# Kernel tuning notes

Hardware: AMD Instinct MI355X
Metric: run time of the kernel (lower is better)

Reference implementation:

```python
import jax, jax.numpy as jnp
import numpy as np

B, N, DIN = 8192, 25, 256
H, F = 8, 32  # heads, per-head dim (output_dim // heads)
E = 48       # directed bone edges
NEG_SLOPE = 0.2


def setup_inputs() -> dict:
    key = jax.random.key(0)
    k0, k1, k2, k3, k4 = jax.random.split(key, 5)
    joint_embeddings = jax.random.normal(k0, (B, N, DIN), dtype=jnp.float32)
    W = jax.random.normal(k1, (DIN, H * F), dtype=jnp.float32) * (1.0 / np.sqrt(DIN))
    a_src = jax.random.normal(k2, (H, F), dtype=jnp.float32) * 0.1
    a_dst = jax.random.normal(k3, (H, F), dtype=jnp.float32) * 0.1
    bias = jnp.zeros((H * F,), dtype=jnp.float32)
    bone_edges = jax.random.randint(k4, (2, E), 0, N, dtype=jnp.int32)
    return {"joint_embeddings": joint_embeddings, "W": W, "a_src": a_src,
            "a_dst": a_dst, "bias": bias, "bone_edges": bone_edges}


def reference(joint_embeddings, W, a_src, a_dst, bias, bone_edges):
    # Linear projection per head: (B, N, H, F)
    h = (joint_embeddings @ W).reshape(B, N, H, F)
    # Per-node attention logits (GATConv splits a into src/dst halves)
    alpha_s = jnp.einsum('bnhf,hf->bnh', h, a_src)  # (B, N, H)
    alpha_d = jnp.einsum('bnhf,hf->bnh', h, a_dst)  # (B, N, H)
    # PyG GATConv default add_self_loops=True
    loops = jnp.arange(N, dtype=bone_edges.dtype)
    src = jnp.concatenate([bone_edges[0], loops])  # (E+N,)
    dst = jnp.concatenate([bone_edges[1], loops])  # (E+N,)
    # Per-edge scores, leaky relu
    e = jax.nn.leaky_relu(alpha_s[:, src] + alpha_d[:, dst], NEG_SLOPE)  # (B, Et, H)
    e_t = jnp.moveaxis(e, 1, 0)  # (Et, B, H) -- segment ops over leading axis
    # Numerically stable segment softmax over incoming edges of each dst node
    m = jax.ops.segment_max(e_t, dst, num_segments=N)  # (N, B, H)
    m = jnp.where(jnp.isfinite(m), m, 0.0)
    ex = jnp.exp(e_t - m[dst])
    denom = jax.ops.segment_sum(ex, dst, num_segments=N)  # (N, B, H)
    alpha = ex / (denom[dst] + 1e-16)  # (Et, B, H)
    # Scatter-aggregate messages
    h_nodes = jnp.moveaxis(h, 1, 0)           # (N, B, H, F)
    msgs = alpha[..., None] * h_nodes[src]     # (Et, B, H, F)
    out = jax.ops.segment_sum(msgs, dst, num_segments=N)  # (N, B, H, F)
    out = jnp.moveaxis(out, 0, 1).reshape(B, N, H * F) + bias
    return out
```

## Files before the change

### kernel.cpp

```cpp
#include <hip/hip_runtime.h>
#include <math.h>

#define NBATCH 8192
#define NNODE  25
#define DIN    256
#define NH     8
#define NF     32
#define HF     256
#define NE     48
#define NT     73
#define NEG_SLOPE 0.2f

#define WS_LNM_OFF 139264

typedef __bf16 bf16x8 __attribute__((ext_vector_type(8)));
typedef float  f32x4  __attribute__((ext_vector_type(4)));

static __device__ __forceinline__ unsigned short f2bf(float f) {
    unsigned int u = __float_as_uint(f);
    return (unsigned short)((u + 0x7fffu + ((u >> 16) & 1u)) >> 16);
}

static __device__ __forceinline__ float bpermf(int idxb, float v) {
    return __int_as_float(__builtin_amdgcn_ds_bpermute(idxb, __float_as_int(v)));
}

__global__ void prep(const float* __restrict__ W,
                     const float* __restrict__ a_src,
                     const float* __restrict__ a_dst,
                     const int*   __restrict__ edges,
                     unsigned short* __restrict__ wf,
                     float* __restrict__ lnm) {
    const int blk = blockIdx.x;
    if (blk < 34) {
        const int tid  = blk * 256 + threadIdx.x;
        const int lane = tid & 63;
        const int ks   = (tid >> 6) & 7;
        const int ct   = tid >> 9;
        const int k0   = ks * 32 + (lane >> 4) * 8;
        if (ct < 16) {
            const int col = ct * 16 + (lane & 15);
#pragma unroll
            for (int j = 0; j < 8; ++j)
                wf[tid * 8 + j] = f2bf(W[(k0 + j) * HF + col]);
        } else {
            const int hp = lane & 15;
            const float* av = (hp < 8) ? (a_src + hp * NF) : (a_dst + (hp - 8) * NF);
            const int wc = (hp & 7) * NF;
#pragma unroll
            for (int j = 0; j < 8; ++j) {
                float s = 0.f;
                for (int f = 0; f < NF; ++f)
                    s = fmaf(W[(k0 + j) * HF + wc + f], av[f], s);
                wf[tid * 8 + j] = f2bf(s);
            }
        }
    } else {
        __shared__ int cnt[32 * 32];
        const int t = threadIdx.x;
        for (int i = t; i < 1024; i += 256) cnt[i] = 0;
        __syncthreads();
        if (t < NT) {
            const int s = (t < NE) ? edges[t]      : (t - NE);
            const int d = (t < NE) ? edges[NE + t] : (t - NE);
            atomicAdd(&cnt[d * 32 + s], 1);
        }
        __syncthreads();
        for (int i = t; i < 1024; i += 256) {
            const int c = cnt[i];
            lnm[i] = (c > 0) ? logf((float)c) : -1e30f;
        }
    }
}

__global__ __launch_bounds__(256, 2)
void gat_wave(const float* __restrict__ X,
              const unsigned short* __restrict__ wf,
              const float* __restrict__ lnm,
              const float* __restrict__ bias,
              float* __restrict__ out)
{
    __shared__ __align__(16) unsigned char sTile[8192];
    const int t   = threadIdx.x;
    const int l   = t & 63;
    const int b   = blockIdx.x * 4 + (t >> 6);
    unsigned char* myT = sTile + (t >> 6) * 2048;
    const int r   = l & 15;
    const int kq  = l >> 4;
    const int kqa = kq & 1;
    const bool hiSel = (kq >> 1) != 0;

    const int idx_as_base = kqa * 32;
    const int idx_ad_base = 128 + r * 4;

    const int wrA = r * 64 + ((kq ^ (r & 6)) << 3);
    const int wrB = r * 64 + (((4 + kq) ^ (r & 6)) << 3);
    const int rdA = r * 64 + (((2 * kq) ^ (r & 6)) << 3);

    bf16x8 af0[8], af1[8];
    const float* Xb = X + (size_t)b * (NNODE * DIN);
    {
        const float* xp0 = Xb + r * DIN + kq * 8;
#pragma unroll
        for (int ks = 0; ks < 8; ++ks) {
            const f32x4 x0 = *(const f32x4*)(xp0 + ks * 32);
            const f32x4 x1 = *(const f32x4*)(xp0 + ks * 32 + 4);
            bf16x8 v;
            v[0]=(__bf16)x0[0]; v[1]=(__bf16)x0[1]; v[2]=(__bf16)x0[2]; v[3]=(__bf16)x0[3];
            v[4]=(__bf16)x1[0]; v[5]=(__bf16)x1[1]; v[6]=(__bf16)x1[2]; v[7]=(__bf16)x1[3];
            af0[ks] = v;
        }
        const bool valid = r < 9;
        const float zm = valid ? 1.f : 0.f;
        const float* xp1 = Xb + (valid ? (16 + r) : r) * DIN + kq * 8;
#pragma unroll
        for (int ks = 0; ks < 8; ++ks) {
            const f32x4 x0 = *(const f32x4*)(xp1 + ks * 32);
            const f32x4 x1 = *(const f32x4*)(xp1 + ks * 32 + 4);
            bf16x8 v;
            v[0]=(__bf16)(x0[0]*zm); v[1]=(__bf16)(x0[1]*zm); v[2]=(__bf16)(x0[2]*zm); v[3]=(__bf16)(x0[3]*zm);
            v[4]=(__bf16)(x1[0]*zm); v[5]=(__bf16)(x1[1]*zm); v[6]=(__bf16)(x1[2]*zm); v[7]=(__bf16)(x1[3]*zm);
            af1[ks] = v;
        }
    }

    f32x4 accL0 = {0.f, 0.f, 0.f, 0.f};
    f32x4 accL1 = {0.f, 0.f, 0.f, 0.f};
#pragma unroll
    for (int ks = 0; ks < 8; ++ks) {
        const bf16x8 wa = *(const bf16x8*)(wf + ((size_t)(128 + ks) * 64 + l) * 8);
        accL0 = __builtin_amdgcn_mfma_f32_16x16x32_bf16(wa, af0[ks], accL0, 0, 0, 0);
        accL1 = __builtin_amdgcn_mfma_f32_16x16x32_bf16(wa, af1[ks], accL1, 0, 0, 0);
    }

    const f32x4 lnA0 = *(const f32x4*)(lnm + r * 32 + kq * 8);
    const f32x4 lnA1 = *(const f32x4*)(lnm + r * 32 + kq * 8 + 4);
    const f32x4 lnB0 = *(const f32x4*)(lnm + (16 + r) * 32 + kq * 8);
    const f32x4 lnB1 = *(const f32x4*)(lnm + (16 + r) * 32 + kq * 8 + 4);

    bf16x8 bwE[8], bwO[8];
#pragma unroll
    for (int ks = 0; ks < 8; ++ks)
        bwE[ks] = *(const bf16x8*)(wf + ((size_t)(0 * 8 + ks) * 64 + l) * 8);
#pragma unroll
    for (int ks = 0; ks < 8; ++ks)
        bwO[ks] = *(const bf16x8*)(wf + ((size_t)(1 * 8 + ks) * 64 + l) * 8);

    float* ob = out + (size_t)b * (NNODE * HF);

#pragma unroll
    for (int h = 0; h < 8; ++h) {
        const int hb2 = (h >> 2) * 64;
        const int q   = h & 3;
        const float ad0 = bpermf(idx_ad_base + hb2, accL0[q]);
        const float ad1 = bpermf(idx_ad_base + hb2, accL1[q]);
        float e0[8], e1[8];
        float s0 = 0.f, s1 = 0.f;
#pragma unroll
        for (int j = 0; j < 8; ++j) {
            const int ia = idx_as_base + hb2 + j * 4;
            const float v0 = bpermf(ia, accL0[q]);
            const float v1 = bpermf(ia, accL1[q]);
            const float asj = hiSel ? v1 : v0;
            const float ln0j = (j < 4) ? lnA0[j & 3] : lnA1[j & 3];
            const float ln1j = (j < 4) ? lnB0[j & 3] : lnB1[j & 3];
            float t0 = asj + ad0; t0 = (t0 > 0.f) ? t0 : NEG_SLOPE * t0;
            float t1 = asj + ad1; t1 = (t1 > 0.f) ? t1 : NEG_SLOPE * t1;
            e0[j] = __expf(t0 + ln0j);
            e1[j] = __expf(t1 + ln1j);
            s0 += e0[j]; s1 += e1[j];
        }
        s0 += __shfl_xor(s0, 16); s0 += __shfl_xor(s0, 32);
        s1 += __shfl_xor(s1, 16); s1 += __shfl_xor(s1, 32);
        const float i0 = 1.f / (s0 + 1e-16f);
        const float i1 = 1.f / (s1 + 1e-16f);
        bf16x8 pf0, pf1;
#pragma unroll
        for (int j = 0; j < 8; ++j) {
            pf0[j] = (__bf16)(e0[j] * i0);
            pf1[j] = (__bf16)(e1[j] * i1);
        }

#pragma unroll
        for (int cc = 0; cc < 2; ++cc) {
            const int ct = 2 * h + cc;
            const bf16x8* bw = cc ? bwO : bwE;
            f32x4 a0 = {0.f, 0.f, 0.f, 0.f};
            f32x4 a1 = {0.f, 0.f, 0.f, 0.f};
#pragma unroll
            for (int ks = 0; ks < 8; ++ks) {
                a0 = __builtin_amdgcn_mfma_f32_16x16x32_bf16(af0[ks], bw[ks], a0, 0, 0, 0);
                a1 = __builtin_amdgcn_mfma_f32_16x16x32_bf16(af1[ks], bw[ks], a1, 0, 0, 0);
            }
            if (h < 7) {
                bf16x8* dst = cc ? bwO : bwE;
#pragma unroll
                for (int ks = 0; ks < 8; ++ks)
                    dst[ks] = *(const bf16x8*)(wf + ((size_t)((ct + 2) * 8 + ks) * 64 + l) * 8);
            }
            unsigned char* buf = myT + ((ct & 1) << 10);
            {
                const unsigned int lo0 = (unsigned int)f2bf(a0[0]) | ((unsigned int)f2bf(a0[1]) << 16);
                const unsigned int hi0 = (unsigned int)f2bf(a0[2]) | ((unsigned int)f2bf(a0[3]) << 16);
                const unsigned int lo1 = (unsigned int)f2bf(a1[0]) | ((unsigned int)f2bf(a1[1]) << 16);
                const unsigned int hi1 = (unsigned int)f2bf(a1[2]) | ((unsigned int)f2bf(a1[3]) << 16);
                *(uint2*)(buf + wrA) = make_uint2(lo0, hi0);
                *(uint2*)(buf + wrB) = make_uint2(lo1, hi1);
            }
            const bf16x8 hb = *(const bf16x8*)(buf + rdA);

            const f32x4 bv = *(const f32x4*)(bias + ct * 16 + kq * 4);
            f32x4 o0 = bv, o1 = bv;
            o0 = __builtin_amdgcn_mfma_f32_16x16x32_bf16(hb, pf0, o0, 0, 0, 0);
            o1 = __builtin_amdgcn_mfma_f32_16x16x32_bf16(hb, pf1, o1, 0, 0, 0);
            *(f32x4*)(ob + r * HF + ct * 16 + kq * 4) = o0;
            if (r < 9)
                *(f32x4*)(ob + (16 + r) * HF + ct * 16 + kq * 4) = o1;
        }
    }
}

extern "C" void kernel_launch(void* const* d_in, const int* in_sizes, int n_in,
                              void* d_out, int out_size, void* d_ws, size_t ws_size,
                              hipStream_t stream) {
    const float* X     = (const float*)d_in[0];
    const float* W     = (const float*)d_in[1];
    const float* a_src = (const float*)d_in[2];
    const float* a_dst = (const float*)d_in[3];
    const float* bias  = (const float*)d_in[4];
    const int*   edges = (const int*)d_in[5];
    float* out = (float*)d_out;
    unsigned short* wf = (unsigned short*)d_ws;
    float* lnm = (float*)((unsigned char*)d_ws + WS_LNM_OFF);

    hipLaunchKernelGGL(prep, dim3(35), dim3(256), 0, stream,
                       W, a_src, a_dst, edges, wf, lnm);
    hipLaunchKernelGGL(gat_wave, dim3(NBATCH / 4), dim3(256), 0, stream,
                       X, wf, lnm, bias, out);
}
```

Baseline: 145.7 us.

## Compute all projection MFMAs upfront before the per-head softmax/aggregation loop

Moves the entire X@W projection for all 16 column tiles into one dense MFMA loop before the per-head loop, packing the results to bf16 in registers (phA/phB). The per-head loop then only stores the precomputed tiles to LDS and does the softmax and aggregation. This removes the interleaved double-buffered weight loads and the serial dependency between the projection MFMAs and the softmax work, so the MFMA pipe runs back to back. The cost is much higher register pressure: 32 f32x4 accumulators plus 32 uint2 values, which risks spills or lower occupancy.

```diff
diff --git a/kernel.cpp b/kernel.cpp
--- a/kernel.cpp
+++ b/kernel.cpp
@@ -124,32 +124,47 @@
         }
     }
 
+    f32x4 acc0[16], acc1[16];
     f32x4 accL0 = {0.f, 0.f, 0.f, 0.f};
     f32x4 accL1 = {0.f, 0.f, 0.f, 0.f};
 #pragma unroll
+    for (int ct = 0; ct < 16; ++ct) {
+        acc0[ct] = f32x4{0.f, 0.f, 0.f, 0.f};
+        acc1[ct] = f32x4{0.f, 0.f, 0.f, 0.f};
+    }
+#pragma unroll
     for (int ks = 0; ks < 8; ++ks) {
+#pragma unroll
+        for (int ct = 0; ct < 16; ++ct) {
+            const bf16x8 bw = *(const bf16x8*)(wf + ((size_t)(ct * 8 + ks) * 64 + l) * 8);
+            acc0[ct] = __builtin_amdgcn_mfma_f32_16x16x32_bf16(af0[ks], bw, acc0[ct], 0, 0, 0);
+            acc1[ct] = __builtin_amdgcn_mfma_f32_16x16x32_bf16(af1[ks], bw, acc1[ct], 0, 0, 0);
+        }
         const bf16x8 wa = *(const bf16x8*)(wf + ((size_t)(128 + ks) * 64 + l) * 8);
         accL0 = __builtin_amdgcn_mfma_f32_16x16x32_bf16(wa, af0[ks], accL0, 0, 0, 0);
         accL1 = __builtin_amdgcn_mfma_f32_16x16x32_bf16(wa, af1[ks], accL1, 0, 0, 0);
     }
 
-    const f32x4 lnA0 = *(const f32x4*)(lnm + r * 32 + kq * 8);
-    const f32x4 lnA1 = *(const f32x4*)(lnm + r * 32 + kq * 8 + 4);
-    const f32x4 lnB0 = *(const f32x4*)(lnm + (16 + r) * 32 + kq * 8);
-    const f32x4 lnB1 = *(const f32x4*)(lnm + (16 + r) * 32 + kq * 8 + 4);
-
-    bf16x8 bwE[8], bwO[8];
-#pragma unroll
-    for (int ks = 0; ks < 8; ++ks)
-        bwE[ks] = *(const bf16x8*)(wf + ((size_t)(0 * 8 + ks) * 64 + l) * 8);
-#pragma unroll
-    for (int ks = 0; ks < 8; ++ks)
-        bwO[ks] = *(const bf16x8*)(wf + ((size_t)(1 * 8 + ks) * 64 + l) * 8);
+    uint2 phA[16], phB[16];
+#pragma unroll
+    for (int ct = 0; ct < 16; ++ct) {
+        phA[ct] = make_uint2(
+            (unsigned int)f2bf(acc0[ct][0]) | ((unsigned int)f2bf(acc0[ct][1]) << 16),
+            (unsigned int)f2bf(acc0[ct][2]) | ((unsigned int)f2bf(acc0[ct][3]) << 16));
+        phB[ct] = make_uint2(
+            (unsigned int)f2bf(acc1[ct][0]) | ((unsigned int)f2bf(acc1[ct][1]) << 16),
+            (unsigned int)f2bf(acc1[ct][2]) | ((unsigned int)f2bf(acc1[ct][3]) << 16));
+    }
 
     float* ob = out + (size_t)b * (NNODE * HF);
 
 #pragma unroll
     for (int h = 0; h < 8; ++h) {
+        const f32x4 lnA0 = *(const f32x4*)(lnm + r * 32 + kq * 8);
+        const f32x4 lnA1 = *(const f32x4*)(lnm + r * 32 + kq * 8 + 4);
+        const f32x4 lnB0 = *(const f32x4*)(lnm + (16 + r) * 32 + kq * 8);
+        const f32x4 lnB1 = *(const f32x4*)(lnm + (16 + r) * 32 + kq * 8 + 4);
+
         const int hb2 = (h >> 2) * 64;
         const int q   = h & 3;
         const float ad0 = bpermf(idx_ad_base + hb2, accL0[q]);
@@ -184,29 +199,9 @@
 #pragma unroll
         for (int cc = 0; cc < 2; ++cc) {
             const int ct = 2 * h + cc;
-            const bf16x8* bw = cc ? bwO : bwE;
-            f32x4 a0 = {0.f, 0.f, 0.f, 0.f};
-            f32x4 a1 = {0.f, 0.f, 0.f, 0.f};
-#pragma unroll
-            for (int ks = 0; ks < 8; ++ks) {
-                a0 = __builtin_amdgcn_mfma_f32_16x16x32_bf16(af0[ks], bw[ks], a0, 0, 0, 0);
-                a1 = __builtin_amdgcn_mfma_f32_16x16x32_bf16(af1[ks], bw[ks], a1, 0, 0, 0);
-            }
-            if (h < 7) {
-                bf16x8* dst = cc ? bwO : bwE;
-#pragma unroll
-                for (int ks = 0; ks < 8; ++ks)
-                    dst[ks] = *(const bf16x8*)(wf + ((size_t)((ct + 2) * 8 + ks) * 64 + l) * 8);
-            }
             unsigned char* buf = myT + ((ct & 1) << 10);
-            {
-                const unsigned int lo0 = (unsigned int)f2bf(a0[0]) | ((unsigned int)f2bf(a0[1]) << 16);
-                const unsigned int hi0 = (unsigned int)f2bf(a0[2]) | ((unsigned int)f2bf(a0[3]) << 16);
-                const unsigned int lo1 = (unsigned int)f2bf(a1[0]) | ((unsigned int)f2bf(a1[1]) << 16);
-                const unsigned int hi1 = (unsigned int)f2bf(a1[2]) | ((unsigned int)f2bf(a1[3]) << 16);
-                *(uint2*)(buf + wrA) = make_uint2(lo0, hi0);
-                *(uint2*)(buf + wrB) = make_uint2(lo1, hi1);
-            }
+            *(uint2*)(buf + wrA) = phA[ct];
+            *(uint2*)(buf + wrB) = phB[ct];
             const bf16x8 hb = *(const bf16x8*)(buf + rdA);
 
             const f32x4 bv = *(const f32x4*)(bias + ct * 16 + kq * 4);
```

Result: slower. 247.2 us (+69.7%).
